# Kernel tuning notes

Hardware: AMD Instinct MI355X
Metric: run time of the kernel (lower is better)

Reference implementation:

```python
import jax, jax.numpy as jnp
import numpy as np

N = 50000
E = 500000
D_DESC = 768; D_TWEET = 768; D_NUM = 5; D_CAT = 3
HID = 128; BLK = 32; CH = 64
CH_HEADS = 8; G_HEADS = 8; G_C = HID // G_HEADS
REL = 2
INV_W = 0.1
SLOPE = 0.01  # nn.LeakyReLU default negative_slope


def leaky(x):
    return jnp.where(x >= 0, x, SLOPE * x)


def _lin(key, din, dout, scale=0.05):
    kw, kb = jax.random.split(key)
    return (jax.random.normal(kw, (din, dout), jnp.float32) * scale,
            jax.random.normal(kb, (dout,), jnp.float32) * scale)


def setup_inputs() -> dict:
    key = jax.random.key(0)
    ks = iter(jax.random.split(key, 64))
    inp = {}
    inp['description'] = jax.random.normal(next(ks), (N, D_DESC), jnp.float32)
    inp['tweet'] = jax.random.normal(next(ks), (N, D_TWEET), jnp.float32)
    inp['num_prop'] = jax.random.normal(next(ks), (N, D_NUM), jnp.float32)
    inp['cat_prop'] = jax.random.normal(next(ks), (N, D_CAT), jnp.float32)
    inp['edge_index'] = jax.random.randint(next(ks), (2, E), 0, N, dtype=jnp.int32)
    inp['edge_type'] = jax.random.randint(next(ks), (E,), 0, REL, dtype=jnp.int32)
    # modality MLPs (weights stored [in,out]; y = x @ W + b)
    inp['W_desc'], inp['b_desc'] = _lin(next(ks), D_DESC, BLK)
    inp['W_tw'], inp['b_tw'] = _lin(next(ks), D_TWEET, BLK)
    inp['W_num'], inp['b_num'] = _lin(next(ks), D_NUM, BLK)
    inp['W_cat'], inp['b_cat'] = _lin(next(ks), D_CAT, BLK)
    # 4 invariant + 4 specific projectors, stacked
    inp['W_inv'] = jax.random.normal(next(ks), (4, BLK, BLK), jnp.float32) * 0.05
    inp['b_inv'] = jax.random.normal(next(ks), (4, BLK), jnp.float32) * 0.05
    inp['W_spec'] = jax.random.normal(next(ks), (4, BLK, BLK), jnp.float32) * 0.05
    inp['b_spec'] = jax.random.normal(next(ks), (4, BLK), jnp.float32) * 0.05
    # channel MultiheadAttention
    inp['W_qkv'] = jax.random.normal(next(ks), (CH, 3 * CH), jnp.float32) * 0.05
    inp['b_qkv'] = jax.random.normal(next(ks), (3 * CH,), jnp.float32) * 0.05
    inp['W_attn_out'], inp['b_attn_out'] = _lin(next(ks), CH, CH)
    inp['ln_g'] = jnp.ones((CH,), jnp.float32)
    inp['ln_b'] = jnp.zeros((CH,), jnp.float32)
    inp['W_c2h'], inp['b_c2h'] = _lin(next(ks), CH, HID)
    inp['rel_emb'] = jax.random.normal(next(ks), (REL, HID), jnp.float32) * 0.05
    # two TransformerConv layers (lin_edge has no bias in PyG)
    for L in ('1', '2'):
        inp['W_q' + L], inp['b_q' + L] = _lin(next(ks), HID, HID)
        inp['W_k' + L], inp['b_k' + L] = _lin(next(ks), HID, HID)
        inp['W_v' + L], inp['b_v' + L] = _lin(next(ks), HID, HID)
        inp['W_e' + L] = jax.random.normal(next(ks), (HID, HID), jnp.float32) * 0.05
        inp['W_skip' + L], inp['b_skip' + L] = _lin(next(ks), HID, HID)
    inp['W_out'], inp['b_out'] = _lin(next(ks), HID, HID)
    inp['W_head'], inp['b_head'] = _lin(next(ks), HID, 2)
    return inp


def transformer_conv(x, src, dst, ea, Wq, bq, Wk, bk, Wv, bv, We, Ws, bs):
    """PyG TransformerConv, concat=True, root_weight=True (inference: no dropout)."""
    n = x.shape[0]
    q = (x @ Wq + bq).reshape(n, G_HEADS, G_C)
    k = (x @ Wk + bk).reshape(n, G_HEADS, G_C)
    v = (x @ Wv + bv).reshape(n, G_HEADS, G_C)
    e = (ea @ We).reshape(-1, G_HEADS, G_C)          # [E,H,C]
    kj = k[src] + e                                   # gather + edge feature
    alpha = (q[dst] * kj).sum(-1) / jnp.sqrt(jnp.float32(G_C))  # [E,H]
    # segment softmax over destination nodes (PyG softmax: denom + 1e-16)
    amax = jax.ops.segment_max(alpha, dst, num_segments=n)
    amax = jnp.where(jnp.isfinite(amax), amax, 0.0)
    ex = jnp.exp(alpha - amax[dst])
    denom = jax.ops.segment_sum(ex, dst, num_segments=n)
    a = ex / (denom[dst] + 1e-16)
    msg = (v[src] + e) * a[..., None]
    out = jax.ops.segment_sum(msg, dst, num_segments=n).reshape(n, G_HEADS * G_C)
    return out + x @ Ws + bs


def reference(description, tweet, num_prop, cat_prop, edge_index, edge_type,
              W_desc, b_desc, W_tw, b_tw, W_num, b_num, W_cat, b_cat,
              W_inv, b_inv, W_spec, b_spec,
              W_qkv, b_qkv, W_attn_out, b_attn_out, ln_g, ln_b,
              W_c2h, b_c2h, rel_emb,
              W_q1, b_q1, W_k1, b_k1, W_v1, b_v1, W_e1, W_skip1, b_skip1,
              W_q2, b_q2, W_k2, b_k2, W_v2, b_v2, W_e2, W_skip2, b_skip2,
              W_out, b_out, W_head, b_head):
    d = leaky(description @ W_desc + b_desc)
    t = leaky(tweet @ W_tw + b_tw)
    nm = leaky(num_prop @ W_num + b_num)
    c = leaky(cat_prop @ W_cat + b_cat)
    m = jnp.stack([d, t, nm, c], axis=1)              # [N,4,BLK]
    inv = jnp.tanh(jnp.einsum('nkb,kbo->nko', m, W_inv) + b_inv)
    spec = leaky(jnp.einsum('nkb,kbo->nko', m, W_spec) + b_spec)
    ch = jnp.concatenate([inv, spec], axis=-1)        # [N,4,CH]
    # channel self-attention (MultiheadAttention, batch_first, inference)
    qkv = ch @ W_qkv + b_qkv
    q, k, v = jnp.split(qkv, 3, axis=-1)
    dh = CH // CH_HEADS
    hs = lambda a: a.reshape(a.shape[0], 4, CH_HEADS, dh)
    scores = jnp.einsum('nqhd,nkhd->nhqk', hs(q), hs(k)) / jnp.sqrt(jnp.float32(dh))
    attn = jax.nn.softmax(scores, axis=-1)
    att = jnp.einsum('nhqk,nkhd->nqhd', attn, hs(v)).reshape(-1, 4, CH)
    att = att @ W_attn_out + b_attn_out
    h = att + ch
    mu = h.mean(-1, keepdims=True)
    var = ((h - mu) ** 2).mean(-1, keepdims=True)
    h = (h - mu) / jnp.sqrt(var + 1e-5) * ln_g + ln_b  # LayerNorm
    fused = leaky(h.mean(1) @ W_c2h + b_c2h)           # [N,HID]
    src, dst = edge_index[0], edge_index[1]
    ea = rel_emb[jnp.clip(edge_type, 0, REL - 1)]      # [E,HID]
    x = transformer_conv(fused, src, dst, ea, W_q1, b_q1, W_k1, b_k1, W_v1, b_v1, W_e1, W_skip1, b_skip1)
    x = leaky(x)
    x = transformer_conv(x, src, dst, ea, W_q2, b_q2, W_k2, b_k2, W_v2, b_v2, W_e2, W_skip2, b_skip2)
    x = leaky(x @ W_out + b_out)
    logits = x @ W_head + b_head
    # auxiliary losses
    center = inv.mean(axis=1, keepdims=True)
    inv_loss = ((inv - center) ** 2).mean()
    norms = jnp.sqrt((spec ** 2).sum(-1))              # [N,4]
    overlap = jnp.float32(0.0)
    for i in range(4):
        for j in range(i + 1, 4):
            cos = (spec[:, i] * spec[:, j]).sum(-1) / jnp.maximum(norms[:, i] * norms[:, j], 1e-8)
            overlap = overlap + jnp.abs(cos).mean()
    overlap = overlap / 6.0
    aux_loss = INV_W * (inv_loss + 0.5 * overlap)
    return logits, aux_loss
```

## Files before the change

kernel.cpp:

```cpp
#include <hip/hip_runtime.h>
#include <hip/hip_bf16.h>
#include <math.h>

#define LEAKY(x) ((x) >= 0.0f ? (x) : 0.01f * (x))

__global__ void k_zero(int* counts, int n) {
  int i = blockIdx.x * 256 + threadIdx.x;
  if (i < n) counts[i] = 0;
}

__global__ void k_count(const int* __restrict__ ei, int* counts, int E) {
  int e = blockIdx.x * 256 + threadIdx.x;
  if (e < E) atomicAdd(&counts[ei[E + e]], 1);
}

__global__ void k_scan1(const int* __restrict__ counts, int* rowst, int* bsums, int N) {
  __shared__ int sd[256];
  int t = threadIdx.x;
  int i = blockIdx.x * 256 + t;
  int v = (i < N) ? counts[i] : 0;
  sd[t] = v;
  __syncthreads();
  for (int off = 1; off < 256; off <<= 1) {
    int add = (t >= off) ? sd[t - off] : 0;
    __syncthreads();
    sd[t] += add;
    __syncthreads();
  }
  if (i < N) rowst[i] = sd[t] - v;
  if (t == 255) bsums[blockIdx.x] = sd[255];
}

__global__ void k_scan2(int* bsums, int NB) {
  __shared__ int sd[256];
  int t = threadIdx.x;
  int v = (t < NB) ? bsums[t] : 0;
  sd[t] = v;
  __syncthreads();
  for (int off = 1; off < 256; off <<= 1) {
    int add = (t >= off) ? sd[t - off] : 0;
    __syncthreads();
    sd[t] += add;
    __syncthreads();
  }
  if (t < NB) bsums[t] = sd[t] - v;
}

__global__ void k_scan3(int* rowst, int* cursor, const int* bsums, int N, int E) {
  int i = blockIdx.x * 256 + threadIdx.x;
  if (i < N) {
    int v = rowst[i] + bsums[i >> 8];
    rowst[i] = v;
    cursor[i] = v;
  }
  if (i == 0) rowst[N] = E;
}

__global__ void k_place(const int* __restrict__ ei, const int* __restrict__ et,
                        int* cursor, unsigned* packed, int E) {
  int e = blockIdx.x * 256 + threadIdx.x;
  if (e < E) {
    int d = ei[E + e];
    int s = ei[e];
    int r = et[e]; r = r < 0 ? 0 : (r > 1 ? 1 : r);
    int pos = atomicAdd(&cursor[d], 1);
    packed[pos] = (unsigned)s | ((unsigned)r << 30);
  }
}

__global__ void k_erel(const float* __restrict__ rel_emb, const float* __restrict__ We1,
                       const float* __restrict__ We2, float* erel) {
  int t = threadIdx.x;
  int layer = t >> 8, r = (t >> 7) & 1, c = t & 127;
  const float* We = layer ? We2 : We1;
  float s = 0.f;
  for (int i = 0; i < 128; i++) s += rel_emb[r * 128 + i] * We[i * 128 + c];
  erel[t] = s;
}

__global__ __launch_bounds__(128) void k_modal(
    const float* __restrict__ desc, const float* __restrict__ tw,
    const float* __restrict__ Wd, const float* __restrict__ bd,
    const float* __restrict__ Wt, const float* __restrict__ bt,
    float* __restrict__ m, int N) {
  __shared__ float As[32][132];
  __shared__ float Bs[32][33];
  int t = threadIdx.x;
  int phase = blockIdx.y;
  const float* Ag = phase ? tw : desc;
  const float* W  = phase ? Wt : Wd;
  const float* bb = phase ? bt : bd;
  int n0 = blockIdx.x * 128;
  int tx = t & 7, ty = t >> 3;
  int tx4 = tx * 4, ty8 = ty * 8;
  float acc[8][4];
#pragma unroll
  for (int i = 0; i < 8; i++)
#pragma unroll
    for (int j = 0; j < 4; j++) acc[i][j] = 0.f;

  for (int kc = 0; kc < 768; kc += 32) {
    __syncthreads();
    {
      int gr = n0 + t; if (gr > N - 1) gr = N - 1;
      const float4* src = (const float4*)(Ag + (size_t)gr * 768 + kc);
#pragma unroll
      for (int q = 0; q < 8; q++) {
        float4 v = src[q];
        As[q * 4 + 0][t] = v.x; As[q * 4 + 1][t] = v.y;
        As[q * 4 + 2][t] = v.z; As[q * 4 + 3][t] = v.w;
      }
      int kr = t >> 2, c8 = (t & 3) * 8;
      const float4* ws4 = (const float4*)(W + (size_t)(kc + kr) * 32 + c8);
      *(float4*)&Bs[kr][c8] = ws4[0];
      *(float4*)&Bs[kr][c8 + 4] = ws4[1];
    }
    __syncthreads();
#pragma unroll 4
    for (int k = 0; k < 32; k++) {
      float4 a0 = *(const float4*)&As[k][ty8];
      float4 a1 = *(const float4*)&As[k][ty8 + 4];
      float4 b0 = *(const float4*)&Bs[k][tx4];
      float a[8] = {a0.x, a0.y, a0.z, a0.w, a1.x, a1.y, a1.z, a1.w};
#pragma unroll
      for (int i = 0; i < 8; i++) {
        acc[i][0] += a[i] * b0.x; acc[i][1] += a[i] * b0.y;
        acc[i][2] += a[i] * b0.z; acc[i][3] += a[i] * b0.w;
      }
    }
  }
  float4 bv = *(const float4*)&bb[tx4];
#pragma unroll
  for (int i = 0; i < 8; i++) {
    int gr = n0 + ty8 + i;
    if (gr < N) {
      float4 v;
      v.x = acc[i][0] + bv.x; v.y = acc[i][1] + bv.y;
      v.z = acc[i][2] + bv.z; v.w = acc[i][3] + bv.w;
      v.x = LEAKY(v.x); v.y = LEAKY(v.y); v.z = LEAKY(v.z); v.w = LEAKY(v.w);
      *(float4*)(m + (size_t)gr * 128 + phase * 32 + tx4) = v;
    }
  }
}

__global__ __launch_bounds__(256) void k_numcat(
    const float* __restrict__ nump, const float* __restrict__ catp,
    const float* __restrict__ Wn, const float* __restrict__ bn,
    const float* __restrict__ Wc, const float* __restrict__ bc,
    float* __restrict__ m, int N) {
  int t = threadIdx.x;
  int n0 = blockIdx.x * 64;
  int c = t & 31, ty = t >> 5;
  float bn_ = bn[c], bc_ = bc[c];
#pragma unroll
  for (int j = 0; j < 8; j++) {
    int gr = n0 + ty * 8 + j;
    int gl = gr > N - 1 ? N - 1 : gr;
    float sn = bn_;
#pragma unroll
    for (int i = 0; i < 5; i++) sn += nump[(size_t)gl * 5 + i] * Wn[i * 32 + c];
    float sc = bc_;
#pragma unroll
    for (int i = 0; i < 3; i++) sc += catp[(size_t)gl * 3 + i] * Wc[i * 32 + c];
    if (gr < N) {
      m[(size_t)gr * 128 + 64 + c] = LEAKY(sn);
      m[(size_t)gr * 128 + 96 + c] = LEAKY(sc);
    }
  }
}

__global__ __launch_bounds__(256) void k_chfuse(
    const float* __restrict__ m, const float* __restrict__ Winv, const float* __restrict__ binv,
    const float* __restrict__ Wspec, const float* __restrict__ bspec,
    float* __restrict__ ch, float* __restrict__ auxp, int N) {
  __shared__ float sm[4][128];
  __shared__ float sch[4][256];
  int t = threadIdx.x;
  int wid = t >> 6, lane = t & 63;
  int n = blockIdx.x * 4 + wid;
  if (n > N - 1) n = N - 1;
  sm[wid][lane] = m[(size_t)n * 128 + lane];
  sm[wid][lane + 64] = m[(size_t)n * 128 + 64 + lane];
  __syncthreads();
#pragma unroll
  for (int p = 0; p < 4; p++) {
    int idx = p * 64 + lane;
    int type = idx >> 7;
    int k = (idx >> 5) & 3;
    int o = idx & 31;
    const float* W = type ? Wspec : Winv;
    const float* bb = type ? bspec : binv;
    float s = bb[k * 32 + o];
    for (int i = 0; i < 32; i++) s += sm[wid][k * 32 + i] * W[(k * 32 + i) * 32 + o];
    float val = type ? LEAKY(s) : tanhf(s);
    sch[wid][k * 64 + type * 32 + o] = val;
  }
  __syncthreads();
  *(float4*)(ch + (size_t)n * 256 + lane * 4) = *(const float4*)&sch[wid][lane * 4];
  float invp = 0.f;
  float pr[10];
#pragma unroll
  for (int q = 0; q < 10; q++) pr[q] = 0.f;
  if (lane < 32) {
    float i0 = sch[wid][lane],       i1 = sch[wid][64 + lane];
    float i2 = sch[wid][128 + lane], i3 = sch[wid][192 + lane];
    float cm = 0.25f * (i0 + i1 + i2 + i3);
    float d0 = i0 - cm, d1 = i1 - cm, d2 = i2 - cm, d3 = i3 - cm;
    invp = d0 * d0 + d1 * d1 + d2 * d2 + d3 * d3;
    float s0 = sch[wid][32 + lane],  s1 = sch[wid][96 + lane];
    float s2 = sch[wid][160 + lane], s3 = sch[wid][224 + lane];
    pr[0] = s0 * s0; pr[1] = s1 * s1; pr[2] = s2 * s2; pr[3] = s3 * s3;
    pr[4] = s0 * s1; pr[5] = s0 * s2; pr[6] = s0 * s3;
    pr[7] = s1 * s2; pr[8] = s1 * s3; pr[9] = s2 * s3;
  }
#pragma unroll
  for (int off = 1; off < 64; off <<= 1) {
    invp += __shfl_xor(invp, off);
#pragma unroll
    for (int q = 0; q < 10; q++) pr[q] += __shfl_xor(pr[q], off);
  }
  if (lane == 0) {
    float n0_ = sqrtf(pr[0]), n1_ = sqrtf(pr[1]), n2_ = sqrtf(pr[2]), n3_ = sqrtf(pr[3]);
    float ov = fabsf(pr[4] / fmaxf(n0_ * n1_, 1e-8f))
             + fabsf(pr[5] / fmaxf(n0_ * n2_, 1e-8f))
             + fabsf(pr[6] / fmaxf(n0_ * n3_, 1e-8f))
             + fabsf(pr[7] / fmaxf(n1_ * n2_, 1e-8f))
             + fabsf(pr[8] / fmaxf(n1_ * n3_, 1e-8f))
             + fabsf(pr[9] / fmaxf(n2_ * n3_, 1e-8f));
    auxp[n] = invp / 128.f + 0.5f * (ov / 6.f);
  }
}

__global__ __launch_bounds__(256) void k_qkvattn(
    const float* __restrict__ ch, const float* __restrict__ Wqkv,
    const float* __restrict__ bqkv, float* __restrict__ att, int N4) {
  __shared__ float As[32][132];
  __shared__ float Bs[32][200];
  __shared__ float qb[128][200];
  int t = threadIdx.x;
  int tok0 = blockIdx.x * 128;
  int tx = t & 15, ty = t >> 4;
  float acc[8][12];
#pragma unroll
  for (int i = 0; i < 8; i++)
#pragma unroll
    for (int j = 0; j < 12; j++) acc[i][j] = 0.f;

  for (int kc = 0; kc < 64; kc += 32) {
    __syncthreads();
    {
      int r = t >> 1, half = t & 1;
      int gtok = tok0 + r; if (gtok > N4 - 1) gtok = N4 - 1;
      const float4* src = (const float4*)(ch + (size_t)gtok * 64 + kc + half * 16);
      int kb = half * 16;
#pragma unroll
      for (int q = 0; q < 4; q++) {
        float4 v = src[q];
        As[kb + q * 4 + 0][r] = v.x; As[kb + q * 4 + 1][r] = v.y;
        As[kb + q * 4 + 2][r] = v.z; As[kb + q * 4 + 3][r] = v.w;
      }
      int kr = t >> 4, cq = (t & 15) * 12;
#pragma unroll
      for (int rr = 0; rr < 2; rr++) {
        int row = kr + rr * 16;
        const float* wsrc = Wqkv + (size_t)(kc + row) * 192 + cq;
        *(float4*)&Bs[row][cq] = *(const float4*)(wsrc);
        *(float4*)&Bs[row][cq + 4] = *(const float4*)(wsrc + 4);
        *(float4*)&Bs[row][cq + 8] = *(const float4*)(wsrc + 8);
      }
    }
    __syncthreads();
#pragma unroll 8
    for (int k = 0; k < 32; k++) {
      float4 a0 = *(const float4*)&As[k][ty * 8];
      float4 a1 = *(const float4*)&As[k][ty * 8 + 4];
      float4 b0 = *(const float4*)&Bs[k][tx * 12];
      float4 b1 = *(const float4*)&Bs[k][tx * 12 + 4];
      float4 b2 = *(const float4*)&Bs[k][tx * 12 + 8];
      float a[8] = {a0.x, a0.y, a0.z, a0.w, a1.x, a1.y, a1.z, a1.w};
      float b[12] = {b0.x, b0.y, b0.z, b0.w, b1.x, b1.y, b1.z, b1.w,
                     b2.x, b2.y, b2.z, b2.w};
#pragma unroll
      for (int i = 0; i < 8; i++)
#pragma unroll
        for (int j = 0; j < 12; j++) acc[i][j] += a[i] * b[j];
    }
  }
  float4 bb0 = *(const float4*)&bqkv[tx * 12];
  float4 bb1 = *(const float4*)&bqkv[tx * 12 + 4];
  float4 bb2 = *(const float4*)&bqkv[tx * 12 + 8];
  __syncthreads();
#pragma unroll
  for (int i = 0; i < 8; i++) {
    int row = ty * 8 + i;
    float4 v0, v1, v2;
    v0.x = acc[i][0] + bb0.x; v0.y = acc[i][1] + bb0.y;
    v0.z = acc[i][2] + bb0.z; v0.w = acc[i][3] + bb0.w;
    v1.x = acc[i][4] + bb1.x; v1.y = acc[i][5] + bb1.y;
    v1.z = acc[i][6] + bb1.z; v1.w = acc[i][7] + bb1.w;
    v2.x = acc[i][8] + bb2.x; v2.y = acc[i][9] + bb2.y;
    v2.z = acc[i][10] + bb2.z; v2.w = acc[i][11] + bb2.w;
    *(float4*)&qb[row][tx * 12] = v0;
    *(float4*)&qb[row][tx * 12 + 4] = v1;
    *(float4*)&qb[row][tx * 12 + 8] = v2;
  }
  __syncthreads();
  {
    int g = t >> 3, h = t & 7;
    int rb = g * 4;
    float kk[4][8], vv[4][8];
#pragma unroll
    for (int j = 0; j < 4; j++)
#pragma unroll
      for (int dd = 0; dd < 8; dd++) {
        kk[j][dd] = qb[rb + j][64 + h * 8 + dd];
        vv[j][dd] = qb[rb + j][128 + h * 8 + dd];
      }
#pragma unroll
    for (int qi = 0; qi < 4; qi++) {
      float qv[8];
#pragma unroll
      for (int dd = 0; dd < 8; dd++) qv[dd] = qb[rb + qi][h * 8 + dd];
      float sc[4];
#pragma unroll
      for (int j = 0; j < 4; j++) {
        float s = 0.f;
#pragma unroll
        for (int dd = 0; dd < 8; dd++) s += qv[dd] * kk[j][dd];
        sc[j] = s * 0.35355339059327373f;
      }
      float mx = fmaxf(fmaxf(sc[0], sc[1]), fmaxf(sc[2], sc[3]));
      float e0 = expf(sc[0] - mx), e1 = expf(sc[1] - mx);
      float e2 = expf(sc[2] - mx), e3 = expf(sc[3] - mx);
      float inv = 1.f / (e0 + e1 + e2 + e3);
      int token = tok0 + rb + qi;
      if (token < N4) {
        float o[8];
#pragma unroll
        for (int dd = 0; dd < 8; dd++)
          o[dd] = (e0 * vv[0][dd] + e1 * vv[1][dd] + e2 * vv[2][dd] + e3 * vv[3][dd]) * inv;
        float* dst = att + (size_t)token * 64 + h * 8;
        float4 w0 = {o[0], o[1], o[2], o[3]};
        float4 w1 = {o[4], o[5], o[6], o[7]};
        *(float4*)(dst) = w0;
        *(float4*)(dst + 4) = w1;
      }
    }
  }
}

__global__ __launch_bounds__(256) void k_attnout(
    const float* __restrict__ att, const float* __restrict__ ch,
    const float* __restrict__ Wao, const float* __restrict__ bao,
    const float* __restrict__ lng, const float* __restrict__ lnb,
    const float* __restrict__ Wc2h, const float* __restrict__ bc2h,
    float* __restrict__ x0, int N, int N4) {
  __shared__ float As[32][132];
  __shared__ float Bs[32][132];
  __shared__ float hmT[64][36];
  int t = threadIdx.x;
  int tok0 = blockIdx.x * 128;
  int tx = t & 15, ty = t >> 4;
  float acc[8][4];
#pragma unroll
  for (int i = 0; i < 8; i++)
#pragma unroll
    for (int j = 0; j < 4; j++) acc[i][j] = 0.f;

  for (int kc = 0; kc < 64; kc += 32) {
    __syncthreads();
    {
      int r = t >> 1, half = t & 1;
      int gtok = tok0 + r; if (gtok > N4 - 1) gtok = N4 - 1;
      const float4* src = (const float4*)(att + (size_t)gtok * 64 + kc + half * 16);
      int kb = half * 16;
#pragma unroll
      for (int q = 0; q < 4; q++) {
        float4 v = src[q];
        As[kb + q * 4 + 0][r] = v.x; As[kb + q * 4 + 1][r] = v.y;
        As[kb + q * 4 + 2][r] = v.z; As[kb + q * 4 + 3][r] = v.w;
      }
      int kr = t >> 3, cq = (t & 7) * 8;
      const float4* wsrc = (const float4*)(Wao + (size_t)(kc + kr) * 64 + cq);
      *(float4*)&Bs[kr][cq] = wsrc[0];
      *(float4*)&Bs[kr][cq + 4] = wsrc[1];
    }
    __syncthreads();
#pragma unroll 8
    for (int k = 0; k < 32; k++) {
      float4 a0 = *(const float4*)&As[k][ty * 8];
      float4 a1 = *(const float4*)&As[k][ty * 8 + 4];
      float4 b0 = *(const float4*)&Bs[k][tx * 4];
      float a[8] = {a0.x, a0.y, a0.z, a0.w, a1.x, a1.y, a1.z, a1.w};
#pragma unroll
      for (int i = 0; i < 8; i++) {
        acc[i][0] += a[i] * b0.x; acc[i][1] += a[i] * b0.y;
        acc[i][2] += a[i] * b0.z; acc[i][3] += a[i] * b0.w;
      }
    }
  }
  float4 bv = *(const float4*)&bao[tx * 4];
  float4 g4 = *(const float4*)&lng[tx * 4];
  float4 lb4 = *(const float4*)&lnb[tx * 4];
  float nv[8][4];
#pragma unroll
  for (int i = 0; i < 8; i++) {
    int row = ty * 8 + i;
    int gtok = tok0 + row; if (gtok > N4 - 1) gtok = N4 - 1;
    float4 c4 = *(const float4*)(ch + (size_t)gtok * 64 + tx * 4);
    float y0 = acc[i][0] + bv.x + c4.x;
    float y1 = acc[i][1] + bv.y + c4.y;
    float y2 = acc[i][2] + bv.z + c4.z;
    float y3 = acc[i][3] + bv.w + c4.w;
    float s1 = y0 + y1 + y2 + y3;
    s1 += __shfl_xor(s1, 1); s1 += __shfl_xor(s1, 2);
    s1 += __shfl_xor(s1, 4); s1 += __shfl_xor(s1, 8);
    float mu = s1 * (1.f / 64.f);
    float d0 = y0 - mu, d1 = y1 - mu, d2 = y2 - mu, d3 = y3 - mu;
    float s2 = d0 * d0 + d1 * d1 + d2 * d2 + d3 * d3;
    s2 += __shfl_xor(s2, 1); s2 += __shfl_xor(s2, 2);
    s2 += __shfl_xor(s2, 4); s2 += __shfl_xor(s2, 8);
    float rs = rsqrtf(s2 * (1.f / 64.f) + 1e-5f);
    nv[i][0] = d0 * rs * g4.x + lb4.x;
    nv[i][1] = d1 * rs * g4.y + lb4.y;
    nv[i][2] = d2 * rs * g4.z + lb4.z;
    nv[i][3] = d3 * rs * g4.w + lb4.w;
  }
#pragma unroll
  for (int ii = 0; ii < 2; ii++) {
    int node = ty * 2 + ii;
#pragma unroll
    for (int j = 0; j < 4; j++) {
      float mval = 0.25f * (nv[ii * 4 + 0][j] + nv[ii * 4 + 1][j]
                          + nv[ii * 4 + 2][j] + nv[ii * 4 + 3][j]);
      hmT[tx * 4 + j][node] = mval;
    }
  }
  int tx2 = t & 31, ty2 = t >> 5;
  float acc2[4][4];
#pragma unroll
  for (int i = 0; i < 4; i++)
#pragma unroll
    for (int j = 0; j < 4; j++) acc2[i][j] = 0.f;
  for (int kc = 0; kc < 64; kc += 32) {
    __syncthreads();
    {
      int kr = t >> 3, cq = (t & 7) * 16;
      const float4* wsrc = (const float4*)(Wc2h + (size_t)(kc + kr) * 128 + cq);
      *(float4*)&Bs[kr][cq] = wsrc[0];
      *(float4*)&Bs[kr][cq + 4] = wsrc[1];
      *(float4*)&Bs[kr][cq + 8] = wsrc[2];
      *(float4*)&Bs[kr][cq + 12] = wsrc[3];
    }
    __syncthreads();
#pragma unroll 8
    for (int kk = 0; kk < 32; kk++) {
      float4 a = *(const float4*)&hmT[kc + kk][ty2 * 4];
      float4 b = *(const float4*)&Bs[kk][tx2 * 4];
      float av[4] = {a.x, a.y, a.z, a.w};
#pragma unroll
      for (int i = 0; i < 4; i++) {
        acc2[i][0] += av[i] * b.x; acc2[i][1] += av[i] * b.y;
        acc2[i][2] += av[i] * b.z; acc2[i][3] += av[i] * b.w;
      }
    }
  }
  float4 bc4 = *(const float4*)&bc2h[tx2 * 4];
  int nb0 = blockIdx.x * 32;
#pragma unroll
  for (int i = 0; i < 4; i++) {
    int gn = nb0 + ty2 * 4 + i;
    if (gn < N) {
      float4 v;
      v.x = acc2[i][0] + bc4.x; v.y = acc2[i][1] + bc4.y;
      v.z = acc2[i][2] + bc4.z; v.w = acc2[i][3] + bc4.w;
      v.x = LEAKY(v.x); v.y = LEAKY(v.y); v.z = LEAKY(v.z); v.w = LEAKY(v.w);
      *(float4*)(x0 + (size_t)gn * 128 + tx2 * 4) = v;
    }
  }
}

__global__ __launch_bounds__(256) void k_gemm(
    const float* __restrict__ x,
    const float* __restrict__ W0, const float* __restrict__ B0,
    const float* __restrict__ W1, const float* __restrict__ B1,
    const float* __restrict__ W2, const float* __restrict__ B2,
    const float* __restrict__ W3, const float* __restrict__ B3,
    float* __restrict__ out, int N, int ostride, int do_leaky) {
  __shared__ float As[32][132];
  __shared__ float Bs[32][132];
  int t = threadIdx.x;
  int cb = blockIdx.y;
  const float* W = (cb == 0) ? W0 : (cb == 1) ? W1 : (cb == 2) ? W2 : W3;
  const float* bias = (cb == 0) ? B0 : (cb == 1) ? B1 : (cb == 2) ? B2 : B3;
  int n0 = blockIdx.x * 128;
  int tx = t & 15, ty = t >> 4;
  int tx4 = tx * 4, ty4 = (ty & 15) * 4;
  float acc[8][8];
#pragma unroll
  for (int i = 0; i < 8; i++)
#pragma unroll
    for (int j = 0; j < 8; j++) acc[i][j] = 0.f;

  for (int kc = 0; kc < 128; kc += 32) {
    __syncthreads();
    {
      int r = t >> 1, half = t & 1;
      int gr = n0 + r; if (gr > N - 1) gr = N - 1;
      const float4* src = (const float4*)(x + (size_t)gr * 128 + kc + half * 16);
      int kb = half * 16;
#pragma unroll
      for (int q = 0; q < 4; q++) {
        float4 v = src[q];
        As[kb + q * 4 + 0][r] = v.x; As[kb + q * 4 + 1][r] = v.y;
        As[kb + q * 4 + 2][r] = v.z; As[kb + q * 4 + 3][r] = v.w;
      }
      int kr = t >> 3, cq = (t & 7) * 16;
      const float4* ws4 = (const float4*)(W + (size_t)(kc + kr) * 128 + cq);
      *(float4*)&Bs[kr][cq] = ws4[0];
      *(float4*)&Bs[kr][cq + 4] = ws4[1];
      *(float4*)&Bs[kr][cq + 8] = ws4[2];
      *(float4*)&Bs[kr][cq + 12] = ws4[3];
    }
    __syncthreads();
#pragma unroll 4
    for (int k = 0; k < 32; k++) {
      float4 a0 = *(const float4*)&As[k][ty4];
      float4 a1 = *(const float4*)&As[k][64 + ty4];
      float4 b0 = *(const float4*)&Bs[k][tx4];
      float4 b1 = *(const float4*)&Bs[k][64 + tx4];
      float a[8] = {a0.x, a0.y, a0.z, a0.w, a1.x, a1.y, a1.z, a1.w};
      float b[8] = {b0.x, b0.y, b0.z, b0.w, b1.x, b1.y, b1.z, b1.w};
#pragma unroll
      for (int i = 0; i < 8; i++)
#pragma unroll
        for (int j = 0; j < 8; j++) acc[i][j] += a[i] * b[j];
    }
  }
  float4 bv0 = *(const float4*)&bias[tx4];
  float4 bv1 = *(const float4*)&bias[64 + tx4];
#pragma unroll
  for (int i = 0; i < 8; i++) {
    int r = (i < 4) ? (ty4 + i) : (60 + ty4 + i);
    int gr = n0 + r;
    if (gr < N) {
      float4 v0, v1;
      v0.x = acc[i][0] + bv0.x; v0.y = acc[i][1] + bv0.y;
      v0.z = acc[i][2] + bv0.z; v0.w = acc[i][3] + bv0.w;
      v1.x = acc[i][4] + bv1.x; v1.y = acc[i][5] + bv1.y;
      v1.z = acc[i][6] + bv1.z; v1.w = acc[i][7] + bv1.w;
      if (do_leaky) {
        v0.x = LEAKY(v0.x); v0.y = LEAKY(v0.y); v0.z = LEAKY(v0.z); v0.w = LEAKY(v0.w);
        v1.x = LEAKY(v1.x); v1.y = LEAKY(v1.y); v1.z = LEAKY(v1.z); v1.w = LEAKY(v1.w);
      }
      float* o = out + (size_t)gr * ostride + (size_t)cb * 128;
      *(float4*)(o + tx4) = v0;
      *(float4*)(o + 64 + tx4) = v1;
    }
  }
}

__global__ __launch_bounds__(256) void k_conv(
    const float* __restrict__ qkvs, const int* __restrict__ rowst,
    const unsigned* __restrict__ packed, const float* __restrict__ erelL,
    float* __restrict__ xout, int N, int do_leaky) {
  __shared__ float se[2][128];
  int t = threadIdx.x;
  se[t >> 7][t & 127] = erelL[t];
  __syncthreads();
  int wid = t >> 6, lane = t & 63;
  int d = blockIdx.x * 4 + wid;
  if (d >= N) return;
  const float* qb = qkvs + (size_t)d * 512;
  float q0 = qb[lane], q1 = qb[64 + lane];
  int e0 = rowst[d], e1 = rowst[d + 1];
  float acc0 = 0.f, acc1 = 0.f, den0 = 0.f, den1 = 0.f;
  for (int e = e0; e < e1; e++) {
    unsigned pk = packed[e];
    int src = pk & 0x0FFFFFFFu;
    int rel = pk >> 30;
    const float* sb = qkvs + (size_t)src * 512;
    float ek0 = se[rel][lane], ek1 = se[rel][64 + lane];
    float k0 = sb[128 + lane] + ek0;
    float k1 = sb[192 + lane] + ek1;
    float v0 = sb[256 + lane] + ek0;
    float v1 = sb[320 + lane] + ek1;
    float p0 = q0 * k0, p1 = q1 * k1;
#pragma unroll
    for (int off = 1; off < 16; off <<= 1) {
      p0 += __shfl_xor(p0, off);
      p1 += __shfl_xor(p1, off);
    }
    float ex0 = expf(p0 * 0.25f);
    float ex1 = expf(p1 * 0.25f);
    acc0 += ex0 * v0; den0 += ex0;
    acc1 += ex1 * v1; den1 += ex1;
  }
  float o0 = acc0 / (den0 + 1e-16f) + qb[384 + lane];
  float o1 = acc1 / (den1 + 1e-16f) + qb[448 + lane];
  if (do_leaky) { o0 = LEAKY(o0); o1 = LEAKY(o1); }
  xout[(size_t)d * 128 + lane] = o0;
  xout[(size_t)d * 128 + 64 + lane] = o1;
}

__global__ __launch_bounds__(256) void k_head(
    const float* __restrict__ x3, const float* __restrict__ Wh,
    const float* __restrict__ bh, float* __restrict__ out, int N) {
  int t = threadIdx.x;
  int node = blockIdx.x * 32 + (t >> 3);
  int l8 = t & 7;
  int gl = node < N ? node : N - 1;
  const float4* xr = (const float4*)(x3 + (size_t)gl * 128 + l8 * 16);
  float h0 = 0.f, h1 = 0.f;
#pragma unroll
  for (int q = 0; q < 4; q++) {
    float4 v = xr[q];
    int kb = (l8 * 16 + q * 4) * 2;
    h0 += v.x * Wh[kb] + v.y * Wh[kb + 2] + v.z * Wh[kb + 4] + v.w * Wh[kb + 6];
    h1 += v.x * Wh[kb + 1] + v.y * Wh[kb + 3] + v.z * Wh[kb + 5] + v.w * Wh[kb + 7];
  }
#pragma unroll
  for (int off = 1; off < 8; off <<= 1) {
    h0 += __shfl_xor(h0, off);
    h1 += __shfl_xor(h1, off);
  }
  if (l8 == 0 && node < N) {
    float2 r; r.x = h0 + bh[0]; r.y = h1 + bh[1];
    *(float2*)(out + (size_t)node * 2) = r;
  }
}

__global__ void k_aux(const float* __restrict__ auxp, float* __restrict__ out, int N) {
  __shared__ float sd[256];
  int t = threadIdx.x;
  float s = 0.f;
  for (int i = t; i < N; i += 256) s += auxp[i];
  sd[t] = s;
  __syncthreads();
  for (int off = 128; off > 0; off >>= 1) {
    if (t < off) sd[t] += sd[t + off];
    __syncthreads();
  }
  if (t == 0) out[0] = 0.1f * sd[0] / (float)N;
}

extern "C" void kernel_launch(void* const* d_in, const int* in_sizes, int n_in,
                              void* d_out, int out_size, void* d_ws, size_t ws_size,
                              hipStream_t stream) {
  (void)n_in; (void)out_size; (void)ws_size;
  const float* desc = (const float*)d_in[0];
  const float* tw   = (const float*)d_in[1];
  const float* nump = (const float*)d_in[2];
  const float* catp = (const float*)d_in[3];
  const int* ei = (const int*)d_in[4];
  const int* et = (const int*)d_in[5];
  const float* Wd = (const float*)d_in[6];  const float* bd = (const float*)d_in[7];
  const float* Wt = (const float*)d_in[8];  const float* bt = (const float*)d_in[9];
  const float* Wn = (const float*)d_in[10]; const float* bn = (const float*)d_in[11];
  const float* Wc = (const float*)d_in[12]; const float* bc = (const float*)d_in[13];
  const float* Winv = (const float*)d_in[14]; const float* binv = (const float*)d_in[15];
  const float* Wspec = (const float*)d_in[16]; const float* bspec = (const float*)d_in[17];
  const float* Wqkv = (const float*)d_in[18]; const float* bqkv = (const float*)d_in[19];
  const float* Wao = (const float*)d_in[20]; const float* bao = (const float*)d_in[21];
  const float* lng = (const float*)d_in[22]; const float* lnb = (const float*)d_in[23];
  const float* Wc2h = (const float*)d_in[24]; const float* bc2h = (const float*)d_in[25];
  const float* rel_emb = (const float*)d_in[26];
  const float* Wq1 = (const float*)d_in[27]; const float* bq1 = (const float*)d_in[28];
  const float* Wk1 = (const float*)d_in[29]; const float* bk1 = (const float*)d_in[30];
  const float* Wv1 = (const float*)d_in[31]; const float* bv1 = (const float*)d_in[32];
  const float* We1 = (const float*)d_in[33];
  const float* Ws1 = (const float*)d_in[34]; const float* bs1 = (const float*)d_in[35];
  const float* Wq2 = (const float*)d_in[36]; const float* bq2 = (const float*)d_in[37];
  const float* Wk2 = (const float*)d_in[38]; const float* bk2 = (const float*)d_in[39];
  const float* Wv2 = (const float*)d_in[40]; const float* bv2 = (const float*)d_in[41];
  const float* We2 = (const float*)d_in[42];
  const float* Ws2 = (const float*)d_in[43]; const float* bs2 = (const float*)d_in[44];
  const float* Wout = (const float*)d_in[45]; const float* bout = (const float*)d_in[46];
  const float* Whead = (const float*)d_in[47]; const float* bhead = (const float*)d_in[48];

  int N = in_sizes[0] / 768;
  int E = in_sizes[5];
  int N4 = N * 4;
  float* out = (float*)d_out;

  float* ws = (float*)d_ws;
  size_t Ns = (size_t)N;
  float* m_buf    = ws;
  float* ch_buf   = m_buf + Ns * 128;
  float* x0_buf   = ch_buf + Ns * 256;
  float* qkvs_buf = x0_buf + Ns * 128;
  float* auxp     = qkvs_buf + Ns * 512;
  float* erel     = auxp + Ns;
  int* counts = (int*)(erel + 512);
  int* rowst  = counts + N;
  int* cursor = rowst + N + 1;
  unsigned* packed = (unsigned*)(cursor + N);
  int* bsums  = (int*)(packed + E);
  float* x1_buf = m_buf;
  float* x2_buf = ch_buf;
  float* x3_buf = x0_buf;
  float* att_buf = qkvs_buf;

  int NB = (N + 255) / 256;
  int EB = (E + 255) / 256;
  int GT = (N + 127) / 128;
  int TT = (N4 + 127) / 128;

  k_zero<<<NB, 256, 0, stream>>>(counts, N);
  k_count<<<EB, 256, 0, stream>>>(ei, counts, E);
  k_scan1<<<NB, 256, 0, stream>>>(counts, rowst, bsums, N);
  k_scan2<<<1, 256, 0, stream>>>(bsums, NB);
  k_scan3<<<NB, 256, 0, stream>>>(rowst, cursor, bsums, N, E);
  k_place<<<EB, 256, 0, stream>>>(ei, et, cursor, packed, E);
  k_erel<<<1, 512, 0, stream>>>(rel_emb, We1, We2, erel);

  k_modal<<<dim3(GT, 2), 128, 0, stream>>>(desc, tw, Wd, bd, Wt, bt, m_buf, N);
  k_numcat<<<(N + 63) / 64, 256, 0, stream>>>(nump, catp, Wn, bn, Wc, bc, m_buf, N);
  k_chfuse<<<(N + 3) / 4, 256, 0, stream>>>(m_buf, Winv, binv, Wspec, bspec,
      ch_buf, auxp, N);
  k_qkvattn<<<TT, 256, 0, stream>>>(ch_buf, Wqkv, bqkv, att_buf, N4);
  k_attnout<<<TT, 256, 0, stream>>>(att_buf, ch_buf, Wao, bao, lng, lnb,
      Wc2h, bc2h, x0_buf, N, N4);

  k_gemm<<<dim3(GT, 4), 256, 0, stream>>>(x0_buf, Wq1, bq1, Wk1, bk1,
      Wv1, bv1, Ws1, bs1, qkvs_buf, N, 512, 0);
  k_conv<<<(N + 3) / 4, 256, 0, stream>>>(qkvs_buf, rowst, packed, erel, x1_buf, N, 1);
  k_gemm<<<dim3(GT, 4), 256, 0, stream>>>(x1_buf, Wq2, bq2, Wk2, bk2,
      Wv2, bv2, Ws2, bs2, qkvs_buf, N, 512, 0);
  k_conv<<<(N + 3) / 4, 256, 0, stream>>>(qkvs_buf, rowst, packed, erel + 256, x2_buf, N, 0);

  k_gemm<<<dim3(GT, 1), 256, 0, stream>>>(x2_buf, Wout, bout, Wout, bout,
      Wout, bout, Wout, bout, x3_buf, N, 128, 1);
  k_head<<<(N + 31) / 32, 256, 0, stream>>>(x3_buf, Whead, bhead, out, N);
  k_aux<<<1, 256, 0, stream>>>(auxp, out + (size_t)2 * N, N);
}
```

Measured before the change: 1.177 ms.

## Halve k_modal row tile and register-prefetch next K chunk

The modality projection GEMM now processes 64 rows per block instead of 128, doubling the grid, and each thread computes a 4x4 instead of an 8x4 output tile. The global loads for the next 32-wide K chunk are issued into registers before the compute loop, so memory latency overlaps the FMAs, and each row is loaded by two threads. This targets the memory-bound streaming of the two 50000x768 inputs through more blocks in flight and software pipelining. The cost is less register-level reuse of each shared-memory load and more blocks re-reading the weight tile.

After: 1.192 ms. Within noise of the previous version (+1.3%).

```diff
diff --git a/kernel.cpp b/kernel.cpp
--- a/kernel.cpp
+++ b/kernel.cpp
@@ -83,47 +83,67 @@
     const float* __restrict__ Wd, const float* __restrict__ bd,
     const float* __restrict__ Wt, const float* __restrict__ bt,
     float* __restrict__ m, int N) {
-  __shared__ float As[32][132];
-  __shared__ float Bs[32][33];
+  __shared__ float As[32][68];
+  __shared__ float Bs[32][36];
   int t = threadIdx.x;
   int phase = blockIdx.y;
   const float* Ag = phase ? tw : desc;
   const float* W  = phase ? Wt : Wd;
   const float* bb = phase ? bt : bd;
-  int n0 = blockIdx.x * 128;
+  int n0 = blockIdx.x * 64;
   int tx = t & 7, ty = t >> 3;
-  int tx4 = tx * 4, ty8 = ty * 8;
-  float acc[8][4];
-#pragma unroll
-  for (int i = 0; i < 8; i++)
+  int tx4 = tx * 4, ty4 = ty * 4;
+
+  int sr = t >> 1, shalf = t & 1;
+  int skr = t >> 2, sc8 = (t & 3) * 8;
+  int gr_ld = n0 + sr; if (gr_ld > N - 1) gr_ld = N - 1;
+  const float* arow = Ag + (size_t)gr_ld * 768 + shalf * 16;
+
+  float acc[4][4];
+#pragma unroll
+  for (int i = 0; i < 4; i++)
 #pragma unroll
     for (int j = 0; j < 4; j++) acc[i][j] = 0.f;
 
-  for (int kc = 0; kc < 768; kc += 32) {
+  float4 ar[4], br[2];
+#pragma unroll
+  for (int q = 0; q < 4; q++) ar[q] = *(const float4*)(arow + q * 4);
+  {
+    const float* wsrc = W + (size_t)skr * 32 + sc8;
+    br[0] = *(const float4*)(wsrc);
+    br[1] = *(const float4*)(wsrc + 4);
+  }
+
+  for (int ck = 0; ck < 24; ck++) {
     __syncthreads();
     {
-      int gr = n0 + t; if (gr > N - 1) gr = N - 1;
-      const float4* src = (const float4*)(Ag + (size_t)gr * 768 + kc);
-#pragma unroll
-      for (int q = 0; q < 8; q++) {
-        float4 v = src[q];
-        As[q * 4 + 0][t] = v.x; As[q * 4 + 1][t] = v.y;
-        As[q * 4 + 2][t] = v.z; As[q * 4 + 3][t] = v.w;
-      }
-      int kr = t >> 2, c8 = (t & 3) * 8;
-      const float4* ws4 = (const float4*)(W + (size_t)(kc + kr) * 32 + c8);
-      *(float4*)&Bs[kr][c8] = ws4[0];
-      *(float4*)&Bs[kr][c8 + 4] = ws4[1];
-    }
-    __syncthreads();
-#pragma unroll 4
+      int kb = shalf * 16;
+#pragma unroll
+      for (int q = 0; q < 4; q++) {
+        float4 v = ar[q];
+        As[kb + q * 4 + 0][sr] = v.x; As[kb + q * 4 + 1][sr] = v.y;
+        As[kb + q * 4 + 2][sr] = v.z; As[kb + q * 4 + 3][sr] = v.w;
+      }
+      *(float4*)&Bs[skr][sc8] = br[0];
+      *(float4*)&Bs[skr][sc8 + 4] = br[1];
+    }
+    if (ck + 1 < 24) {
+      int kc = (ck + 1) * 32;
+      const float* an = arow + kc;
+#pragma unroll
+      for (int q = 0; q < 4; q++) ar[q] = *(const float4*)(an + q * 4);
+      const float* wsrc = W + (size_t)(kc + skr) * 32 + sc8;
+      br[0] = *(const float4*)(wsrc);
+      br[1] = *(const float4*)(wsrc + 4);
+    }
+    __syncthreads();
+#pragma unroll 8
     for (int k = 0; k < 32; k++) {
-      float4 a0 = *(const float4*)&As[k][ty8];
-      float4 a1 = *(const float4*)&As[k][ty8 + 4];
+      float4 a0 = *(const float4*)&As[k][ty4];
       float4 b0 = *(const float4*)&Bs[k][tx4];
-      float a[8] = {a0.x, a0.y, a0.z, a0.w, a1.x, a1.y, a1.z, a1.w};
-#pragma unroll
-      for (int i = 0; i < 8; i++) {
+      float a[4] = {a0.x, a0.y, a0.z, a0.w};
+#pragma unroll
+      for (int i = 0; i < 4; i++) {
         acc[i][0] += a[i] * b0.x; acc[i][1] += a[i] * b0.y;
         acc[i][2] += a[i] * b0.z; acc[i][3] += a[i] * b0.w;
       }
@@ -131,8 +151,8 @@
   }
   float4 bv = *(const float4*)&bb[tx4];
 #pragma unroll
-  for (int i = 0; i < 8; i++) {
-    int gr = n0 + ty8 + i;
+  for (int i = 0; i < 4; i++) {
+    int gr = n0 + ty4 + i;
     if (gr < N) {
       float4 v;
       v.x = acc[i][0] + bv.x; v.y = acc[i][1] + bv.y;
@@ -704,6 +724,7 @@
   int NB = (N + 255) / 256;
   int EB = (E + 255) / 256;
   int GT = (N + 127) / 128;
+  int MT = (N + 63) / 64;
   int TT = (N4 + 127) / 128;
 
   k_zero<<<NB, 256, 0, stream>>>(counts, N);
@@ -714,7 +735,7 @@
   k_place<<<EB, 256, 0, stream>>>(ei, et, cursor, packed, E);
   k_erel<<<1, 512, 0, stream>>>(rel_emb, We1, We2, erel);
 
-  k_modal<<<dim3(GT, 2), 128, 0, stream>>>(desc, tw, Wd, bd, Wt, bt, m_buf, N);
+  k_modal<<<dim3(MT, 2), 128, 0, stream>>>(desc, tw, Wd, bd, Wt, bt, m_buf, N);
   k_numcat<<<(N + 63) / 64, 256, 0, stream>>>(nump, catp, Wn, bn, Wc, bc, m_buf, N);
   k_chfuse<<<(N + 3) / 4, 256, 0, stream>>>(m_buf, Winv, binv, Wspec, bspec,
       ch_buf, auxp, N);
```
